# Kernel tuning notes

Measured on AMD Instinct MI355X. Metric: run time of the kernel, lower is better.

## Reference

```python
import jax, jax.numpy as jnp
import numpy as np

B, T, A, P = 128, 128, 16, 4
D, H, Q, QI, V = 256, 512, 128, 512, 64
NUM_TRICKS = 13
SIGNAL_PHASE = 1
# static phase routing: contiguous blocks of T/P positions per phase (phase_mask buffer)
PHASE_ID = (np.arange(T) * P // T).astype(np.int32)
_DECAY = 0.6
_nt_left = NUM_TRICKS - np.arange(NUM_TRICKS, dtype=np.float32)
P_SIGNAL = ((1.0 - _DECAY) / (1.0 - _DECAY ** _nt_left)).astype(np.float32)


def setup_inputs() -> dict:
    key = jax.random.key(0)
    ks = jax.random.split(key, 12)
    a = jax.random.randint(ks[0], (B, T, A, 3), 0, V, dtype=jnp.int32)
    pad = (jax.random.uniform(ks[1], (B, T, A)) < 0.3) & (jnp.arange(A) >= 1)
    valid_actions = jnp.where(pad[..., None], -1, a)
    phase = jnp.broadcast_to(jnp.asarray(PHASE_ID), (B, T)).astype(jnp.int32)
    trick = jax.random.randint(ks[2], (B, T), 0, NUM_TRICKS, dtype=jnp.int32)
    backbone_embed = jax.random.normal(ks[3], (B, T, QI), jnp.float32)
    s = lambda k, shape, fan: jax.random.normal(k, shape, jnp.float32) / np.float32(np.sqrt(fan))
    return dict(
        backbone_embed=backbone_embed, valid_actions=valid_actions, phase=phase, trick=trick,
        emb0=s(ks[4], (V, D), D), emb1=s(ks[5], (V, D), D), emb2=s(ks[6], (V, D), D),
        ln_g=jnp.ones((D,), jnp.float32), ln_b=jnp.zeros((D,), jnp.float32),
        kW1=s(ks[7], (P, D, H), D), kb1=jnp.zeros((P, H), jnp.float32),
        kW2=s(ks[8], (P, H, H), H), kb2=jnp.zeros((P, H), jnp.float32),
        kW3=s(ks[9], (P, H, Q), H), kb3=jnp.zeros((P, Q), jnp.float32),
        qW=s(ks[10], (P, QI, Q), QI), qb=jnp.zeros((P, Q), jnp.float32),
    )


def _forward(backbone_embed, valid_actions, phase, trick,
             emb0, emb1, emb2, ln_g, ln_b,
             kW1, kb1, kW2, kb2, kW3, kb3, qW, qb):
    pid = PHASE_ID  # static (T,) routing -> gather per-position phase params (same math as mask gather/scatter)
    idx = jnp.clip(valid_actions, 0, V - 1)
    x = emb0[idx[..., 0]] + emb1[idx[..., 1]] + emb2[idx[..., 2]]  # (B,T,A,D) action embed
    mu = jnp.mean(x, -1, keepdims=True)
    var = jnp.var(x, -1, keepdims=True)
    x = (x - mu) * jax.lax.rsqrt(var + 1e-5) * ln_g + ln_b  # key LayerNorm
    # phase-branched key MLP (BranchedFF over MLP)
    h = jax.nn.relu(jnp.einsum('btad,tdh->btah', x, kW1[pid]) + kb1[pid][None, :, None, :])
    h = jax.nn.relu(jnp.einsum('btah,thg->btag', h, kW2[pid]) + kb2[pid][None, :, None, :])
    keyv = jnp.einsum('btah,thq->btaq', h, kW3[pid]) + kb3[pid][None, :, None, :]  # (B,T,A,Q)
    # phase-branched query Linear (BranchedFF over Linear)
    query = jnp.einsum('btd,tdq->btq', backbone_embed, qW[pid]) + qb[pid][None]  # (B,T,Q)
    attn = jnp.einsum('btq,btaq->bta', query, keyv) / np.float32(np.sqrt(Q))
    invalid = valid_actions[..., 0] == -1
    attn = jnp.where(invalid, -jnp.inf, attn)
    # no-signal log-weight
    n_valid = jnp.sum(~invalid, -1).astype(attn.dtype)  # (B,T)
    p_s = jnp.asarray(P_SIGNAL)[trick]
    wgt = jnp.log(jnp.maximum((1.0 - p_s) / p_s * (n_valid - 1.0), 1e-5))
    wgt = jnp.where(n_valid == 1.0, 0.0, wgt)
    attn = attn.at[..., 0].add(jnp.where(phase == SIGNAL_PHASE, wgt, 0.0))
    return jax.nn.log_softmax(attn, axis=-1)


def reference(backbone_embed, valid_actions, phase, trick,
              emb0, emb1, emb2, ln_g, ln_b,
              kW1, kb1, kW2, kb2, kW3, kb3, qW, qb):
    return _forward(backbone_embed, valid_actions, phase, trick,
                    emb0, emb1, emb2, ln_g, ln_b,
                    kW1, kb1, kW2, kb2, kW3, kb3, qW, qb)
```

## Files before the change

kernel.cpp:

```cpp
#include <hip/hip_runtime.h>
#include <hip/hip_bf16.h>
#include <cmath>

constexpr int Bc = 128, Tc = 128, Ac = 16;
constexpr int Dc = 256, Hc = 512, Qc = 128, QIc = 512, Vc = 64, NTk = 13;
constexpr float NEG_BIG = -1e30f;
constexpr float ACT_SCALE = 16.f;
constexpr float ACC_SCALE = 1.f / 256.f;
constexpr float ACC_TO_ACT = 1.f / 16.f;

typedef unsigned int uint;
typedef uint uint2v __attribute__((ext_vector_type(2)));
typedef int i32x8 __attribute__((ext_vector_type(8)));
typedef float f32x4 __attribute__((ext_vector_type(4)));

#define MFMA128(a, b, c) __builtin_amdgcn_mfma_scale_f32_16x16x128_f8f6f4( \
    (a), (b), (c), 0, 0, 0, 0x7F7F7F7F, 0, 0x7F7F7F7F)

__device__ __forceinline__ unsigned short f2bfu(float f) {
  __hip_bfloat16 h = __float2bfloat16(f);
  return *(unsigned short*)&h;
}
__device__ __forceinline__ float bf2f(short s) {
  return __uint_as_float(((unsigned)(unsigned short)s) << 16);
}
__device__ __forceinline__ uint pack4_fp8(float a, float b, float c, float d) {
  uint v = 0;
  v = __builtin_amdgcn_cvt_pk_fp8_f32(a, b, v, 0);
  v = __builtin_amdgcn_cvt_pk_fp8_f32(c, d, v, 1);
  return v;
}

__global__ void transform_all(const float* __restrict__ kW1, const float* __restrict__ kW2,
                              const float* __restrict__ kW3, const float* __restrict__ qW,
                              int* __restrict__ kW1f, int* __restrict__ kW2f,
                              int* __restrict__ kW3f, int* __restrict__ qWf) {
  int gid = blockIdx.x * 256 + threadIdx.x;
  const float* W;
  int* dst;
  int NT, KC, N, local;
  if (gid < 16384) {
    W = kW1; dst = kW1f; NT = 32; KC = 2; N = 512; local = gid;
  } else if (gid < 49152) {
    W = kW2; dst = kW2f; NT = 32; KC = 4; N = 512; local = gid - 16384;
  } else if (gid < 57344) {
    W = kW3; dst = kW3f; NT = 8; KC = 4; N = 128; local = gid - 49152;
  } else {
    W = qW; dst = qWf; NT = 8; KC = 4; N = 128; local = gid - 57344;
  }
  int lane = local & 63;
  int frag = local >> 6;
  int kc = frag % KC;
  int rest = frag / KC;
  int nt = rest % NT;
  int pp = rest / NT;
  int K = KC * 128;
  int n = nt * 16 + (lane & 15);
  int k0 = kc * 128 + (lane >> 4) * 32;
  const float* src = W + ((size_t)pp * K + k0) * N + n;
  i32x8 v;
#pragma unroll
  for (int jj = 0; jj < 8; ++jj) {
    float f0 = src[(size_t)(4 * jj + 0) * N] * ACT_SCALE;
    float f1 = src[(size_t)(4 * jj + 1) * N] * ACT_SCALE;
    float f2 = src[(size_t)(4 * jj + 2) * N] * ACT_SCALE;
    float f3 = src[(size_t)(4 * jj + 3) * N] * ACT_SCALE;
    v[jj] = (int)pack4_fp8(f0, f1, f2, f3);
  }
  *(i32x8*)(dst + (size_t)local * 8) = v;
}

template <int KC, int WT, int AT, bool RELU, int OUTMODE, int SIN, int SOUT, int CMASK>
__device__ __forceinline__ void layer128(
    const char* __restrict__ aB, void* __restrict__ o0,
    const int* __restrict__ Wfi, const float* __restrict__ bias,
    int wt0, int lane) {
  const int c = lane & 15, q = lane >> 4;
  const int sw = (c & 1) << 4;
  const char* ap = aB + (c & CMASK) * SIN + q * 32;

#define LDB(kc_, at_) ({                                        \
    const char* pa_ = ap + (at_) * 16 * SIN + (kc_) * 128;      \
    uint4 u0_ = *(const uint4*)(pa_ + sw);                      \
    uint4 u1_ = *(const uint4*)(pa_ + (16 ^ sw));               \
    i32x8 bv_;                                                  \
    bv_[0] = (int)u0_.x; bv_[1] = (int)u0_.y;                   \
    bv_[2] = (int)u0_.z; bv_[3] = (int)u0_.w;                   \
    bv_[4] = (int)u1_.x; bv_[5] = (int)u1_.y;                   \
    bv_[6] = (int)u1_.z; bv_[7] = (int)u1_.w; bv_; })
#define LDW(wt_, kc_) \
    (*(const i32x8*)(Wfi + ((size_t)((wt0 + (wt_)) * KC + (kc_))) * 512 + lane * 8))

  f32x4 acc[WT][AT];
#pragma unroll
  for (int wt = 0; wt < WT; ++wt)
#pragma unroll
    for (int at = 0; at < AT; ++at)
#pragma unroll
      for (int r = 0; r < 4; ++r) acc[wt][at][r] = 0.f;

  i32x8 bfA, bfB;
  bfA = LDB(0, 0);

  if constexpr (KC * WT <= 4) {
    i32x8 wv[KC][WT];
#pragma unroll
    for (int kc = 0; kc < KC; ++kc)
#pragma unroll
      for (int wt = 0; wt < WT; ++wt) wv[kc][wt] = LDW(wt, kc);
#pragma unroll
    for (int kc = 0; kc < KC; ++kc) {
#pragma unroll
      for (int at = 0; at < AT; ++at) {
        const int f = kc * AT + at;
        const int nf = f + 1;
        if ((f & 1) == 0) {
          if (nf < KC * AT) bfB = LDB(nf / AT, nf % AT);
#pragma unroll
          for (int wt = 0; wt < WT; ++wt)
            acc[wt][at] = MFMA128(wv[kc][wt], bfA, acc[wt][at]);
        } else {
          if (nf < KC * AT) bfA = LDB(nf / AT, nf % AT);
#pragma unroll
          for (int wt = 0; wt < WT; ++wt)
            acc[wt][at] = MFMA128(wv[kc][wt], bfB, acc[wt][at]);
        }
      }
      __builtin_amdgcn_sched_barrier(0);
    }
  } else {
    i32x8 wvA[WT], wvB[WT];
#pragma unroll
    for (int wt = 0; wt < WT; ++wt) wvA[wt] = LDW(wt, 0);
#pragma unroll
    for (int kc = 0; kc < KC; ++kc) {
      const bool ke = (kc & 1) == 0;
      if (kc + 1 < KC) {
#pragma unroll
        for (int wt = 0; wt < WT; ++wt) {
          if (ke) wvB[wt] = LDW(wt, kc + 1);
          else    wvA[wt] = LDW(wt, kc + 1);
        }
      }
#pragma unroll
      for (int at = 0; at < AT; ++at) {
        const int f = kc * AT + at;
        const int nf = f + 1;
        if ((f & 1) == 0) {
          if (nf < KC * AT) bfB = LDB(nf / AT, nf % AT);
#pragma unroll
          for (int wt = 0; wt < WT; ++wt)
            acc[wt][at] = MFMA128(ke ? wvA[wt] : wvB[wt], bfA, acc[wt][at]);
        } else {
          if (nf < KC * AT) bfA = LDB(nf / AT, nf % AT);
#pragma unroll
          for (int wt = 0; wt < WT; ++wt)
            acc[wt][at] = MFMA128(ke ? wvA[wt] : wvB[wt], bfB, acc[wt][at]);
        }
      }
      __builtin_amdgcn_sched_barrier(0);
    }
  }
#undef LDB
#undef LDW

#pragma unroll
  for (int wt = 0; wt < WT; ++wt) {
    const int nb = (wt0 + wt) * 16 + 4 * q;
    float4 bv = *(const float4*)(bias + nb);
#pragma unroll
    for (int at = 0; at < AT; ++at) {
      const int row = at * 16 + c;
      if (OUTMODE == 0) {
        float s0 = fmaf(acc[wt][at][0], ACC_TO_ACT, bv.x * ACT_SCALE);
        float s1 = fmaf(acc[wt][at][1], ACC_TO_ACT, bv.y * ACT_SCALE);
        float s2 = fmaf(acc[wt][at][2], ACC_TO_ACT, bv.z * ACT_SCALE);
        float s3 = fmaf(acc[wt][at][3], ACC_TO_ACT, bv.w * ACT_SCALE);
        if (RELU) {
          s0 = fmaxf(s0, 0.f); s1 = fmaxf(s1, 0.f);
          s2 = fmaxf(s2, 0.f); s3 = fmaxf(s3, 0.f);
        }
        *(uint*)((char*)o0 + row * SOUT + (nb ^ sw)) = pack4_fp8(s0, s1, s2, s3);
      } else if (OUTMODE == 1) {
        float s0 = fmaf(acc[wt][at][0], ACC_SCALE, bv.x);
        float s1 = fmaf(acc[wt][at][1], ACC_SCALE, bv.y);
        float s2 = fmaf(acc[wt][at][2], ACC_SCALE, bv.z);
        float s3 = fmaf(acc[wt][at][3], ACC_SCALE, bv.w);
        uint2v u;
        u.x = ((uint)f2bfu(s1) << 16) | f2bfu(s0);
        u.y = ((uint)f2bfu(s3) << 16) | f2bfu(s2);
        *(uint2v*)((short*)o0 + row * SOUT + nb) = u;
      } else {
        if (c < 4) {
          float4 st;
          st.x = fmaf(acc[wt][at][0], ACC_SCALE, bv.x);
          st.y = fmaf(acc[wt][at][1], ACC_SCALE, bv.y);
          st.z = fmaf(acc[wt][at][2], ACC_SCALE, bv.z);
          st.w = fmaf(acc[wt][at][3], ACC_SCALE, bv.w);
          *(float4*)((float*)o0 + c * SOUT + nb) = st;
        }
      }
    }
  }
}

constexpr int SX = 288;
constexpr int SH = 544;
constexpr int SKV = 136;
constexpr int SQY = 132;

__global__ __launch_bounds__(512, 4) void policy_main(
    const float* __restrict__ be, const int* __restrict__ va,
    const int* __restrict__ phase, const int* __restrict__ trick,
    const float* __restrict__ emb0, const float* __restrict__ emb1,
    const float* __restrict__ emb2, const float* __restrict__ ln_g,
    const float* __restrict__ ln_b,
    const float* __restrict__ kb1, const float* __restrict__ kb2,
    const float* __restrict__ kb3, const float* __restrict__ qb,
    const int* __restrict__ kW1f, const int* __restrict__ kW2f,
    const int* __restrict__ kW3f, const int* __restrict__ qWf,
    float* __restrict__ out) {
  __shared__ __align__(16) char bufA[64 * SH];
  __shared__ __align__(16) char bufB[64 * SH];
  __shared__ __align__(16) char beAb[4 * SH];
  __shared__ __align__(16) float QYs[4 * SQY];
  __shared__ float attn_s[64];
  __shared__ int inval_s[64];
  __shared__ int ph_s[4], tr_s[4];

  char* Xs = bufA;
  char* H2 = bufA;
  char* H1 = bufB;
  short* KV = (short*)bufB;

  const int tid = threadIdx.x;
  const int lane = tid & 63;
  const int wu = __builtin_amdgcn_readfirstlane(tid >> 6);
  const int p = blockIdx.x & 3;
  const int g = blockIdx.x >> 2;
  const int b = g >> 3;
  const int t0 = p * 32 + (g & 7) * 4;
  const int bt0 = b * Tc + t0;

  if (tid < 64) {
    inval_s[tid] = (va[((size_t)bt0 * Ac + tid) * 3] == -1);
  } else if (tid < 68) {
    ph_s[tid - 64] = phase[bt0 + tid - 64];
  } else if (tid < 72) {
    tr_s[tid - 68] = trick[bt0 + tid - 68];
  }
  if (tid < 128) {
    const int tok = tid >> 5, li = tid & 31;
    const float4* bp4 = (const float4*)(be + ((size_t)(bt0 + tok)) * QIc + li * 16);
    float4 a0 = bp4[0], a1 = bp4[1], a2 = bp4[2], a3 = bp4[3];
    uint4 v;
    v.x = pack4_fp8(a0.x * ACT_SCALE, a0.y * ACT_SCALE, a0.z * ACT_SCALE, a0.w * ACT_SCALE);
    v.y = pack4_fp8(a1.x * ACT_SCALE, a1.y * ACT_SCALE, a1.z * ACT_SCALE, a1.w * ACT_SCALE);
    v.z = pack4_fp8(a2.x * ACT_SCALE, a2.y * ACT_SCALE, a2.z * ACT_SCALE, a2.w * ACT_SCALE);
    v.w = pack4_fp8(a3.x * ACT_SCALE, a3.y * ACT_SCALE, a3.z * ACT_SCALE, a3.w * ACT_SCALE);
    *(uint4*)(beAb + tok * SH + ((li * 16) ^ ((tok & 1) << 4))) = v;
  }
  {
    const int r = tid >> 3, part = tid & 7, d0 = part * 32;
    const int* vp = va + ((size_t)bt0 * Ac + r) * 3;
    int i0 = min(max(vp[0], 0), Vc - 1);
    int i1 = min(max(vp[1], 0), Vc - 1);
    int i2 = min(max(vp[2], 0), Vc - 1);
    const float4* e0 = (const float4*)(emb0 + i0 * Dc + d0);
    const float4* e1 = (const float4*)(emb1 + i1 * Dc + d0);
    const float4* e2 = (const float4*)(emb2 + i2 * Dc + d0);
    float xv[32];
    float sum = 0.f, ss = 0.f;
#pragma unroll
    for (int j = 0; j < 8; ++j) {
      float4 v0 = e0[j], v1 = e1[j], v2 = e2[j];
      float4 v;
      v.x = v0.x + v1.x + v2.x; v.y = v0.y + v1.y + v2.y;
      v.z = v0.z + v1.z + v2.z; v.w = v0.w + v1.w + v2.w;
      xv[j * 4 + 0] = v.x; xv[j * 4 + 1] = v.y; xv[j * 4 + 2] = v.z; xv[j * 4 + 3] = v.w;
      sum += v.x + v.y + v.z + v.w;
      ss += v.x * v.x + v.y * v.y + v.z * v.z + v.w * v.w;
    }
    sum += __shfl_xor(sum, 1); sum += __shfl_xor(sum, 2); sum += __shfl_xor(sum, 4);
    ss += __shfl_xor(ss, 1);   ss += __shfl_xor(ss, 2);   ss += __shfl_xor(ss, 4);
    const float mu = sum / (float)Dc;
    const float rstd = rsqrtf(ss / (float)Dc - mu * mu + 1e-5f);
    uint dw[8];
#pragma unroll
    for (int j = 0; j < 8; ++j) {
      float4 gg = *(const float4*)(ln_g + d0 + 4 * j);
      float4 bb = *(const float4*)(ln_b + d0 + 4 * j);
      float y0 = ((xv[4 * j + 0] - mu) * rstd * gg.x + bb.x) * ACT_SCALE;
      float y1 = ((xv[4 * j + 1] - mu) * rstd * gg.y + bb.y) * ACT_SCALE;
      float y2 = ((xv[4 * j + 2] - mu) * rstd * gg.z + bb.z) * ACT_SCALE;
      float y3 = ((xv[4 * j + 3] - mu) * rstd * gg.w + bb.w) * ACT_SCALE;
      dw[j] = pack4_fp8(y0, y1, y2, y3);
    }
    uint4 lo, hi;
    lo.x = dw[0]; lo.y = dw[1]; lo.z = dw[2]; lo.w = dw[3];
    hi.x = dw[4]; hi.y = dw[5]; hi.z = dw[6]; hi.w = dw[7];
    const int swr = (r & 1) << 4;
    *(uint4*)(Xs + r * SX + (d0 ^ swr)) = lo;
    *(uint4*)(Xs + r * SX + ((d0 + 16) ^ swr)) = hi;
  }
  __syncthreads();

  layer128<2, 2, 4, true, 0, SX, SH, 15>(Xs, H1, kW1f + (size_t)p * 32768,
                                         kb1 + p * Hc, wu * 2, lane);
  layer128<4, 1, 1, false, 2, SH, SQY, 3>(beAb, (void*)QYs, qWf + (size_t)p * 16384,
                                          qb + p * Qc, wu, lane);
  layer128<2, 2, 4, true, 0, SX, SH, 15>(Xs, H1, kW1f + (size_t)p * 32768,
                                         kb1 + p * Hc, 16 + wu * 2, lane);
  __syncthreads();

  layer128<4, 2, 4, true, 0, SH, SH, 15>(H1, H2, kW2f + (size_t)p * 65536,
                                         kb2 + p * Hc, wu * 2, lane);
  layer128<4, 2, 4, true, 0, SH, SH, 15>(H1, H2, kW2f + (size_t)p * 65536,
                                         kb2 + p * Hc, 16 + wu * 2, lane);
  __syncthreads();

  layer128<4, 1, 4, false, 1, SH, SKV, 15>(H2, (void*)KV, kW3f + (size_t)p * 16384,
                                           kb3 + p * Qc, wu, lane);
  __syncthreads();

  {
    const int r = tid >> 3, part = tid & 7, tok = r >> 4;
    const uint2v* kpu = (const uint2v*)(KV + r * SKV + part * 16);
    const float4* qp4 = (const float4*)(QYs + tok * SQY + part * 16);
    float s = 0.f;
#pragma unroll
    for (int j = 0; j < 4; ++j) {
      uint2v kk = kpu[j];
      float4 qq = qp4[j];
      s += bf2f((short)(kk.x & 0xffff)) * qq.x;
      s += bf2f((short)(kk.x >> 16)) * qq.y;
      s += bf2f((short)(kk.y & 0xffff)) * qq.z;
      s += bf2f((short)(kk.y >> 16)) * qq.w;
    }
    s += __shfl_xor(s, 1); s += __shfl_xor(s, 2); s += __shfl_xor(s, 4);
    if (part == 0) attn_s[r] = s * 0.08838834764831845f;
  }
  __syncthreads();

  if (tid < 4) {
    const int tok = tid;
    const int bt = bt0 + tok;
    float av[Ac];
    int nv = 0;
#pragma unroll
    for (int a = 0; a < Ac; ++a) {
      int iv = inval_s[tok * Ac + a];
      nv += iv ? 0 : 1;
      av[a] = iv ? NEG_BIG : attn_s[tok * Ac + a];
    }
    if (ph_s[tok] == 1) {
      const int nt = NTk - tr_s[tok];
      float dp = 1.f;
      for (int i = 0; i < nt; ++i) dp *= 0.6f;
      const float ps = 0.4f / (1.f - dp);
      float wgt = (nv == 1) ? 0.f : logf(fmaxf((1.f - ps) / ps * ((float)nv - 1.f), 1e-5f));
      av[0] += wgt;
    }
    float m = NEG_BIG;
#pragma unroll
    for (int a = 0; a < Ac; ++a) m = fmaxf(m, av[a]);
    float s = 0.f;
#pragma unroll
    for (int a = 0; a < Ac; ++a) s += expf(av[a] - m);
    const float lse = logf(s) + m;
#pragma unroll
    for (int a = 0; a < Ac; ++a)
      out[bt * Ac + a] = inval_s[tok * Ac + a] ? NEG_BIG : (av[a] - lse);
  }
}

extern "C" void kernel_launch(void* const* d_in, const int* in_sizes, int n_in,
                              void* d_out, int out_size, void* d_ws, size_t ws_size,
                              hipStream_t stream) {
  const float* be   = (const float*)d_in[0];
  const int*   va   = (const int*)d_in[1];
  const int*   ph   = (const int*)d_in[2];
  const int*   tr   = (const int*)d_in[3];
  const float* emb0 = (const float*)d_in[4];
  const float* emb1 = (const float*)d_in[5];
  const float* emb2 = (const float*)d_in[6];
  const float* lng  = (const float*)d_in[7];
  const float* lnb  = (const float*)d_in[8];
  const float* kW1  = (const float*)d_in[9];
  const float* kb1  = (const float*)d_in[10];
  const float* kW2  = (const float*)d_in[11];
  const float* kb2  = (const float*)d_in[12];
  const float* kW3  = (const float*)d_in[13];
  const float* kb3  = (const float*)d_in[14];
  const float* qW   = (const float*)d_in[15];
  const float* qb   = (const float*)d_in[16];
  float* out = (float*)d_out;

  int* kW1f = (int*)d_ws;
  int* kW2f = kW1f + 131072;
  int* kW3f = kW2f + 262144;
  int* qWf  = kW3f + 65536;

  transform_all<<<256, 256, 0, stream>>>(kW1, kW2, kW3, qW, kW1f, kW2f, kW3f, qWf);

  policy_main<<<4096, 512, 0, stream>>>(be, va, ph, tr, emb0, emb1, emb2, lng, lnb,
                                        kb1, kb2, kb3, qb, kW1f, kW2f, kW3f, qWf, out);
}
```

Baseline: 345.5 us.

## Switch key MLP layers to 32x32x64 FP8 MFMA with matching weight layout

The three key-MLP layers move from 16x16x128 scaled FP8 MFMA to 32x32x64 MFMA tiles. Weights are pre-packed into a matching fragment layout, and the transform kernel now runs twice as many threads, each writing half a fragment. The XOR swizzle on shared-memory activation rows is dropped and row strides are narrowed to fit the new access pattern. The larger tiles should raise operand reuse and cut the number of MFMA and LDS instructions per block, at the cost of more accumulator registers and possible LDS bank conflicts without the swizzle.

Measured after the change: 348.6 us. About the same (+0.9%).

```diff
diff --git a/kernel.cpp b/kernel.cpp
--- a/kernel.cpp
+++ b/kernel.cpp
@@ -13,8 +13,11 @@
 typedef uint uint2v __attribute__((ext_vector_type(2)));
 typedef int i32x8 __attribute__((ext_vector_type(8)));
 typedef float f32x4 __attribute__((ext_vector_type(4)));
+typedef float f32x16 __attribute__((ext_vector_type(16)));
 
 #define MFMA128(a, b, c) __builtin_amdgcn_mfma_scale_f32_16x16x128_f8f6f4( \
+    (a), (b), (c), 0, 0, 0, 0x7F7F7F7F, 0, 0x7F7F7F7F)
+#define MFMA32(a, b, c) __builtin_amdgcn_mfma_scale_f32_32x32x64_f8f6f4( \
     (a), (b), (c), 0, 0, 0, 0x7F7F7F7F, 0, 0x7F7F7F7F)
 
 __device__ __forceinline__ unsigned short f2bfu(float f) {
@@ -35,18 +38,21 @@
                               const float* __restrict__ kW3, const float* __restrict__ qW,
                               int* __restrict__ kW1f, int* __restrict__ kW2f,
                               int* __restrict__ kW3f, int* __restrict__ qWf) {
-  int gid = blockIdx.x * 256 + threadIdx.x;
+  int id = blockIdx.x * 256 + threadIdx.x;
+  int jh = id >> 16;
+  int gid = id & 65535;
   const float* W;
   int* dst;
   int NT, KC, N, local;
+  bool big;
   if (gid < 16384) {
-    W = kW1; dst = kW1f; NT = 32; KC = 2; N = 512; local = gid;
+    W = kW1; dst = kW1f; NT = 16; KC = 4; N = 512; local = gid; big = true;
   } else if (gid < 49152) {
-    W = kW2; dst = kW2f; NT = 32; KC = 4; N = 512; local = gid - 16384;
+    W = kW2; dst = kW2f; NT = 16; KC = 8; N = 512; local = gid - 16384; big = true;
   } else if (gid < 57344) {
-    W = kW3; dst = kW3f; NT = 8; KC = 4; N = 128; local = gid - 49152;
+    W = kW3; dst = kW3f; NT = 4; KC = 8; N = 128; local = gid - 49152; big = true;
   } else {
-    W = qW; dst = qWf; NT = 8; KC = 4; N = 128; local = gid - 57344;
+    W = qW; dst = qWf; NT = 8; KC = 4; N = 128; local = gid - 57344; big = false;
   }
   int lane = local & 63;
   int frag = local >> 6;
@@ -54,20 +60,113 @@
   int rest = frag / KC;
   int nt = rest % NT;
   int pp = rest / NT;
-  int K = KC * 128;
-  int n = nt * 16 + (lane & 15);
-  int k0 = kc * 128 + (lane >> 4) * 32;
+  int K = KC * (big ? 64 : 128);
+  int n, k0;
+  if (big) { n = nt * 32 + (lane & 31); k0 = kc * 64 + (lane >> 5) * 32; }
+  else     { n = nt * 16 + (lane & 15); k0 = kc * 128 + (lane >> 4) * 32; }
+  k0 += jh * 16;
   const float* src = W + ((size_t)pp * K + k0) * N + n;
-  i32x8 v;
-#pragma unroll
-  for (int jj = 0; jj < 8; ++jj) {
+  int4 v;
+  int vv[4];
+#pragma unroll
+  for (int jj = 0; jj < 4; ++jj) {
     float f0 = src[(size_t)(4 * jj + 0) * N] * ACT_SCALE;
     float f1 = src[(size_t)(4 * jj + 1) * N] * ACT_SCALE;
     float f2 = src[(size_t)(4 * jj + 2) * N] * ACT_SCALE;
     float f3 = src[(size_t)(4 * jj + 3) * N] * ACT_SCALE;
-    v[jj] = (int)pack4_fp8(f0, f1, f2, f3);
-  }
-  *(i32x8*)(dst + (size_t)local * 8) = v;
+    vv[jj] = (int)pack4_fp8(f0, f1, f2, f3);
+  }
+  v.x = vv[0]; v.y = vv[1]; v.z = vv[2]; v.w = vv[3];
+  *(int4*)(dst + (size_t)local * 8 + jh * 4) = v;
+}
+
+template <int KC, int WT, int AT, bool RELU, int OUTMODE, int SIN, int SOUT>
+__device__ __forceinline__ void layer32(
+    const char* __restrict__ aB, void* __restrict__ o0,
+    const int* __restrict__ Wfi, const float* __restrict__ bias,
+    int nt0, int lane) {
+  const int row = lane & 31, q = lane >> 5;
+  const char* ap = aB + row * SIN + q * 32;
+
+#define LDB32(kc_, at_) ({                                      \
+    const char* pa_ = ap + (at_) * 32 * SIN + (kc_) * 64;       \
+    uint4 u0_ = *(const uint4*)(pa_);                           \
+    uint4 u1_ = *(const uint4*)(pa_ + 16);                      \
+    i32x8 bv_;                                                  \
+    bv_[0] = (int)u0_.x; bv_[1] = (int)u0_.y;                   \
+    bv_[2] = (int)u0_.z; bv_[3] = (int)u0_.w;                   \
+    bv_[4] = (int)u1_.x; bv_[5] = (int)u1_.y;                   \
+    bv_[6] = (int)u1_.z; bv_[7] = (int)u1_.w; bv_; })
+#define LDW32(wt_, kc_) \
+    (*(const i32x8*)(Wfi + ((size_t)((nt0 + (wt_)) * KC + (kc_))) * 512 + lane * 8))
+
+  f32x16 acc[WT][AT];
+#pragma unroll
+  for (int wt = 0; wt < WT; ++wt)
+#pragma unroll
+    for (int at = 0; at < AT; ++at)
+#pragma unroll
+      for (int r = 0; r < 16; ++r) acc[wt][at][r] = 0.f;
+
+  i32x8 wvA[WT], wvB[WT];
+#pragma unroll
+  for (int wt = 0; wt < WT; ++wt) wvA[wt] = LDW32(wt, 0);
+
+#pragma unroll
+  for (int kc = 0; kc < KC; ++kc) {
+    const bool ke = (kc & 1) == 0;
+    if (kc + 1 < KC) {
+#pragma unroll
+      for (int wt = 0; wt < WT; ++wt) {
+        if (ke) wvB[wt] = LDW32(wt, kc + 1);
+        else    wvA[wt] = LDW32(wt, kc + 1);
+      }
+    }
+#pragma unroll
+    for (int at = 0; at < AT; ++at) {
+      i32x8 bf = LDB32(kc, at);
+#pragma unroll
+      for (int wt = 0; wt < WT; ++wt)
+        acc[wt][at] = MFMA32(ke ? wvA[wt] : wvB[wt], bf, acc[wt][at]);
+    }
+    __builtin_amdgcn_sched_barrier(0);
+  }
+#undef LDB32
+#undef LDW32
+
+#pragma unroll
+  for (int wt = 0; wt < WT; ++wt) {
+    const int tb = (nt0 + wt) * 32 + 4 * q;
+#pragma unroll
+    for (int at = 0; at < AT; ++at) {
+      const int rowout = at * 32 + row;
+#pragma unroll
+      for (int j = 0; j < 4; ++j) {
+        const int nb = tb + 8 * j;
+        float4 bv = *(const float4*)(bias + nb);
+        if (OUTMODE == 0) {
+          float s0 = fmaf(acc[wt][at][4 * j + 0], ACC_TO_ACT, bv.x * ACT_SCALE);
+          float s1 = fmaf(acc[wt][at][4 * j + 1], ACC_TO_ACT, bv.y * ACT_SCALE);
+          float s2 = fmaf(acc[wt][at][4 * j + 2], ACC_TO_ACT, bv.z * ACT_SCALE);
+          float s3 = fmaf(acc[wt][at][4 * j + 3], ACC_TO_ACT, bv.w * ACT_SCALE);
+          if (RELU) {
+            s0 = fmaxf(s0, 0.f); s1 = fmaxf(s1, 0.f);
+            s2 = fmaxf(s2, 0.f); s3 = fmaxf(s3, 0.f);
+          }
+          *(uint*)((char*)o0 + rowout * SOUT + nb) = pack4_fp8(s0, s1, s2, s3);
+        } else {
+          float s0 = fmaf(acc[wt][at][4 * j + 0], ACC_SCALE, bv.x);
+          float s1 = fmaf(acc[wt][at][4 * j + 1], ACC_SCALE, bv.y);
+          float s2 = fmaf(acc[wt][at][4 * j + 2], ACC_SCALE, bv.z);
+          float s3 = fmaf(acc[wt][at][4 * j + 3], ACC_SCALE, bv.w);
+          uint2v u;
+          u.x = ((uint)f2bfu(s1) << 16) | f2bfu(s0);
+          u.y = ((uint)f2bfu(s3) << 16) | f2bfu(s2);
+          *(uint2v*)((short*)o0 + rowout * SOUT + nb) = u;
+        }
+      }
+    }
+  }
 }
 
 template <int KC, int WT, int AT, bool RELU, int OUTMODE, int SIN, int SOUT, int CMASK>
@@ -102,64 +201,30 @@
   i32x8 bfA, bfB;
   bfA = LDB(0, 0);
 
-  if constexpr (KC * WT <= 4) {
-    i32x8 wv[KC][WT];
-#pragma unroll
-    for (int kc = 0; kc < KC; ++kc)
-#pragma unroll
-      for (int wt = 0; wt < WT; ++wt) wv[kc][wt] = LDW(wt, kc);
-#pragma unroll
-    for (int kc = 0; kc < KC; ++kc) {
-#pragma unroll
-      for (int at = 0; at < AT; ++at) {
-        const int f = kc * AT + at;
-        const int nf = f + 1;
-        if ((f & 1) == 0) {
-          if (nf < KC * AT) bfB = LDB(nf / AT, nf % AT);
-#pragma unroll
-          for (int wt = 0; wt < WT; ++wt)
-            acc[wt][at] = MFMA128(wv[kc][wt], bfA, acc[wt][at]);
-        } else {
-          if (nf < KC * AT) bfA = LDB(nf / AT, nf % AT);
-#pragma unroll
-          for (int wt = 0; wt < WT; ++wt)
-            acc[wt][at] = MFMA128(wv[kc][wt], bfB, acc[wt][at]);
-        }
+  i32x8 wv[KC][WT];
+#pragma unroll
+  for (int kc = 0; kc < KC; ++kc)
+#pragma unroll
+    for (int wt = 0; wt < WT; ++wt) wv[kc][wt] = LDW(wt, kc);
+#pragma unroll
+  for (int kc = 0; kc < KC; ++kc) {
+#pragma unroll
+    for (int at = 0; at < AT; ++at) {
+      const int f = kc * AT + at;
+      const int nf = f + 1;
+      if ((f & 1) == 0) {
+        if (nf < KC * AT) bfB = LDB(nf / AT, nf % AT);
+#pragma unroll
+        for (int wt = 0; wt < WT; ++wt)
+          acc[wt][at] = MFMA128(wv[kc][wt], bfA, acc[wt][at]);
+      } else {
+        if (nf < KC * AT) bfA = LDB(nf / AT, nf % AT);
+#pragma unroll
+        for (int wt = 0; wt < WT; ++wt)
+          acc[wt][at] = MFMA128(wv[kc][wt], bfB, acc[wt][at]);
       }
-      __builtin_amdgcn_sched_barrier(0);
-    }
-  } else {
-    i32x8 wvA[WT], wvB[WT];
-#pragma unroll
-    for (int wt = 0; wt < WT; ++wt) wvA[wt] = LDW(wt, 0);
-#pragma unroll
-    for (int kc = 0; kc < KC; ++kc) {
-      const bool ke = (kc & 1) == 0;
-      if (kc + 1 < KC) {
-#pragma unroll
-        for (int wt = 0; wt < WT; ++wt) {
-          if (ke) wvB[wt] = LDW(wt, kc + 1);
-          else    wvA[wt] = LDW(wt, kc + 1);
-        }
-      }
-#pragma unroll
-      for (int at = 0; at < AT; ++at) {
-        const int f = kc * AT + at;
-        const int nf = f + 1;
-        if ((f & 1) == 0) {
-          if (nf < KC * AT) bfB = LDB(nf / AT, nf % AT);
-#pragma unroll
-          for (int wt = 0; wt < WT; ++wt)
-            acc[wt][at] = MFMA128(ke ? wvA[wt] : wvB[wt], bfA, acc[wt][at]);
-        } else {
-          if (nf < KC * AT) bfA = LDB(nf / AT, nf % AT);
-#pragma unroll
-          for (int wt = 0; wt < WT; ++wt)
-            acc[wt][at] = MFMA128(ke ? wvA[wt] : wvB[wt], bfB, acc[wt][at]);
-        }
-      }
-      __builtin_amdgcn_sched_barrier(0);
-    }
+    }
+    __builtin_amdgcn_sched_barrier(0);
   }
 #undef LDB
 #undef LDW
@@ -170,27 +235,7 @@
     float4 bv = *(const float4*)(bias + nb);
 #pragma unroll
     for (int at = 0; at < AT; ++at) {
-      const int row = at * 16 + c;
-      if (OUTMODE == 0) {
-        float s0 = fmaf(acc[wt][at][0], ACC_TO_ACT, bv.x * ACT_SCALE);
-        float s1 = fmaf(acc[wt][at][1], ACC_TO_ACT, bv.y * ACT_SCALE);
-        float s2 = fmaf(acc[wt][at][2], ACC_TO_ACT, bv.z * ACT_SCALE);
-        float s3 = fmaf(acc[wt][at][3], ACC_TO_ACT, bv.w * ACT_SCALE);
-        if (RELU) {
-          s0 = fmaxf(s0, 0.f); s1 = fmaxf(s1, 0.f);
-          s2 = fmaxf(s2, 0.f); s3 = fmaxf(s3, 0.f);
-        }
-        *(uint*)((char*)o0 + row * SOUT + (nb ^ sw)) = pack4_fp8(s0, s1, s2, s3);
-      } else if (OUTMODE == 1) {
-        float s0 = fmaf(acc[wt][at][0], ACC_SCALE, bv.x);
-        float s1 = fmaf(acc[wt][at][1], ACC_SCALE, bv.y);
-        float s2 = fmaf(acc[wt][at][2], ACC_SCALE, bv.z);
-        float s3 = fmaf(acc[wt][at][3], ACC_SCALE, bv.w);
-        uint2v u;
-        u.x = ((uint)f2bfu(s1) << 16) | f2bfu(s0);
-        u.y = ((uint)f2bfu(s3) << 16) | f2bfu(s2);
-        *(uint2v*)((short*)o0 + row * SOUT + nb) = u;
-      } else {
+      if (OUTMODE == 2) {
         if (c < 4) {
           float4 st;
           st.x = fmaf(acc[wt][at][0], ACC_SCALE, bv.x);
@@ -204,8 +249,9 @@
   }
 }
 
-constexpr int SX = 288;
-constexpr int SH = 544;
+constexpr int SX = 272;
+constexpr int SH = 528;
+constexpr int SBE = 544;
 constexpr int SKV = 136;
 constexpr int SQY = 132;
 
@@ -222,7 +268,7 @@
     float* __restrict__ out) {
   __shared__ __align__(16) char bufA[64 * SH];
   __shared__ __align__(16) char bufB[64 * SH];
-  __shared__ __align__(16) char beAb[4 * SH];
+  __shared__ __align__(16) char beAb[4 * SBE];
   __shared__ __align__(16) float QYs[4 * SQY];
   __shared__ float attn_s[64];
   __shared__ int inval_s[64];
@@ -258,7 +304,7 @@
     v.y = pack4_fp8(a1.x * ACT_SCALE, a1.y * ACT_SCALE, a1.z * ACT_SCALE, a1.w * ACT_SCALE);
     v.z = pack4_fp8(a2.x * ACT_SCALE, a2.y * ACT_SCALE, a2.z * ACT_SCALE, a2.w * ACT_SCALE);
     v.w = pack4_fp8(a3.x * ACT_SCALE, a3.y * ACT_SCALE, a3.z * ACT_SCALE, a3.w * ACT_SCALE);
-    *(uint4*)(beAb + tok * SH + ((li * 16) ^ ((tok & 1) << 4))) = v;
+    *(uint4*)(beAb + tok * SBE + ((li * 16) ^ ((tok & 1) << 4))) = v;
   }
   {
     const int r = tid >> 3, part = tid & 7, d0 = part * 32;
@@ -299,28 +345,25 @@
     uint4 lo, hi;
     lo.x = dw[0]; lo.y = dw[1]; lo.z = dw[2]; lo.w = dw[3];
     hi.x = dw[4]; hi.y = dw[5]; hi.z = dw[6]; hi.w = dw[7];
-    const int swr = (r & 1) << 4;
-    *(uint4*)(Xs + r * SX + (d0 ^ swr)) = lo;
-    *(uint4*)(Xs + r * SX + ((d0 + 16) ^ swr)) = hi;
+    *(uint4*)(Xs + r * SX + d0) = lo;
+    *(uint4*)(Xs + r * SX + d0 + 16) = hi;
   }
   __syncthreads();
 
-  layer128<2, 2, 4, true, 0, SX, SH, 15>(Xs, H1, kW1f + (size_t)p * 32768,
-                                         kb1 + p * Hc, wu * 2, lane);
-  layer128<4, 1, 1, false, 2, SH, SQY, 3>(beAb, (void*)QYs, qWf + (size_t)p * 16384,
-                                          qb + p * Qc, wu, lane);
-  layer128<2, 2, 4, true, 0, SX, SH, 15>(Xs, H1, kW1f + (size_t)p * 32768,
-                                         kb1 + p * Hc, 16 + wu * 2, lane);
+  layer32<4, 2, 2, true, 0, SX, SH>(Xs, H1, kW1f + (size_t)p * 32768,
+                                    kb1 + p * Hc, wu * 2, lane);
+  layer128<4, 1, 1, false, 2, SBE, SQY, 3>(beAb, (void*)QYs, qWf + (size_t)p * 16384,
+                                           qb + p * Qc, wu, lane);
   __syncthreads();
 
-  layer128<4, 2, 4, true, 0, SH, SH, 15>(H1, H2, kW2f + (size_t)p * 65536,
-                                         kb2 + p * Hc, wu * 2, lane);
-  layer128<4, 2, 4, true, 0, SH, SH, 15>(H1, H2, kW2f + (size_t)p * 65536,
-                                         kb2 + p * Hc, 16 + wu * 2, lane);
+  layer32<8, 2, 2, true, 0, SH, SH>(H1, H2, kW2f + (size_t)p * 65536,
+                                    kb2 + p * Hc, wu * 2, lane);
   __syncthreads();
 
-  layer128<4, 1, 4, false, 1, SH, SKV, 15>(H2, (void*)KV, kW3f + (size_t)p * 16384,
-                                           kb3 + p * Qc, wu, lane);
+  layer32<8, 1, 1, false, 1, SH, SKV>(H2 + (wu & 1) * 32 * SH,
+                                      (void*)(KV + (wu & 1) * 32 * SKV),
+                                      kW3f + (size_t)p * 16384,
+                                      kb3 + p * Qc, wu >> 1, lane);
   __syncthreads();
 
   {
@@ -401,7 +444,7 @@
   int* kW3f = kW2f + 262144;
   int* qWf  = kW3f + 65536;
 
-  transform_all<<<256, 256, 0, stream>>>(kW1, kW2, kW3, qW, kW1f, kW2f, kW3f, qWf);
+  transform_all<<<512, 256, 0, stream>>>(kW1, kW2, kW3, qW, kW1f, kW2f, kW3f, qWf);
 
   policy_main<<<4096, 512, 0, stream>>>(be, va, ph, tr, emb0, emb1, emb2, lng, lnb,
                                         kb1, kb2, kb3, qb, kW1f, kW2f, kW3f, qWf, out);
```
